# Performance work log

Hardware: AMD Instinct MI355X
Metric: run time of the kernel (lower is better)

The kernel has to match this reference:

```python
import jax, jax.numpy as jnp
import numpy as np

N_Q_HEADS = 16
N_KV_HEADS = 4
HEAD_DIM = 128
SLIDING_WINDOW = 1024
ROPE_BASE = 1024


def _rope_tables(L, dim):
    # half-truncate RoPE: first dim//4 freqs geometric, next dim//4 zero
    freqs = (1.0 / ROPE_BASE) ** jnp.linspace(0.0, 1.0, num=dim // 4)
    freqs = jnp.concatenate([freqs, jnp.zeros(dim // 4, dtype=freqs.dtype)])
    theta = jnp.arange(L, dtype=jnp.float32)[:, None] * freqs[None, :]  # (L, dim/2)
    cos = jnp.cos(theta)[None, :, None, :]  # (1, L, 1, dim/2)
    sin = jnp.sin(theta)[None, :, None, :]
    return cos, sin


def _rotate(x, cos, sin):
    # x: (B, L, H, D)
    x1, x2 = jnp.split(x, 2, axis=-1)
    return jnp.concatenate([x1 * cos + x2 * sin, -x1 * sin + x2 * cos], axis=-1)


def setup_inputs() -> dict:
    key = jax.random.key(0)
    k1, k2, k3, k4 = jax.random.split(key, 4)
    B, L, D = 1, 2048, 2048
    qkv_dim = (N_Q_HEADS + 2 * N_KV_HEADS) * HEAD_DIM  # 3072
    return {
        "x": jax.random.normal(k1, (B, L, D), dtype=jnp.float32),
        "Wqkv": jax.random.normal(k2, (D, qkv_dim), dtype=jnp.float32) * (D ** -0.5),
        "Wo": jax.random.normal(k3, (N_Q_HEADS * HEAD_DIM, D), dtype=jnp.float32) * ((N_Q_HEADS * HEAD_DIM) ** -0.5),
        "s": jax.random.normal(k4, (1, N_Q_HEADS), dtype=jnp.float32) * 0.1,
    }


def reference(x, Wqkv, Wo, s):
    B, L, D = x.shape
    H, QM, hd = N_KV_HEADS, N_Q_HEADS // N_KV_HEADS, HEAD_DIM

    proj = x @ Wqkv  # (B, L, (Hq + 2*Hkv) * hd)
    q, k, v = jnp.split(proj, (N_Q_HEADS * hd, (N_Q_HEADS + N_KV_HEADS) * hd), axis=-1)

    cos, sin = _rope_tables(L, hd)
    q = _rotate(q.reshape(B, L, -1, hd), cos, sin).reshape(B, L, H, QM, hd)
    k = _rotate(k.reshape(B, L, H, hd), cos, sin)
    v = v.reshape(B, L, H, hd)

    sm_scale = 1.0 / jnp.sqrt(jnp.float32(hd))
    q_pos = jnp.arange(L)[None, :, None]
    k_pos = jnp.arange(L)[None, None, :]
    causal = q_pos >= k_pos                       # (1, L, L)
    window = q_pos < k_pos + SLIDING_WINDOW       # index % 2 == 0 -> window active
    mask = causal & window

    # (B, H, M, Lq, Lk) attention logits
    attn = jnp.einsum("bqhmd,bkhd->bhmqk", q, k) * sm_scale
    # NOTE: faithful to source: -inf placed WHERE mask is True
    attn = jnp.where(mask, -jnp.inf, attn)

    sink = jnp.broadcast_to(s.reshape(B, H, QM, 1, 1), (B, H, QM, L, 1))
    w = jax.nn.softmax(jnp.concatenate([attn, sink], axis=-1), axis=-1)[..., :-1]

    out = jnp.einsum("bhmqk,bkhd->bqhmd", w, v).reshape(B, L, -1)
    return out @ Wo
```

## Files before the change

kernel.cpp:

```cpp
#include <hip/hip_runtime.h>
#include <hip/hip_bf16.h>
#include <math.h>

typedef __bf16 bf16;
typedef __bf16 bf16x8 __attribute__((ext_vector_type(8)));
typedef __bf16 bf16x4v __attribute__((ext_vector_type(4)));
typedef short s16x4 __attribute__((ext_vector_type(4)));
typedef float f32x4 __attribute__((ext_vector_type(4)));

#define GLD16(gp, lp) __builtin_amdgcn_global_load_lds( \
    (__attribute__((address_space(1))) void*)(void*)(gp), \
    (__attribute__((address_space(3))) void*)(lp), 16, 0, 0)

#define L_SEQ 2048
#define D_MODEL 2048
#define QKV_N 3072
#define HD 128
#define QSCALE 0.1275310242959836f
#define LOG2E 1.4426950408889634f

__global__ __launch_bounds__(256) void prep(const float* __restrict__ x,
                                            const float* __restrict__ Wqkv,
                                            const float* __restrict__ Wo,
                                            bf16* __restrict__ xb,
                                            bf16* __restrict__ wqkvT,
                                            bf16* __restrict__ woT) {
    __shared__ float tile[32][33];
    int bid = blockIdx.x;
    if (bid < 4096) {
        int idx = (bid * 256 + threadIdx.x) * 4;
        float4 f = *(const float4*)(x + idx);
        bf16x4v o;
        o.x = (bf16)f.x; o.y = (bf16)f.y; o.z = (bf16)f.z; o.w = (bf16)f.w;
        *(bf16x4v*)(xb + idx) = o;
        return;
    }
    bid -= 4096;
    const float* src; bf16* dst; long ld_s, ld_d; int bx, by;
    if (bid < 6144) { bx = bid % 96; by = bid / 96; src = Wqkv; dst = wqkvT; ld_s = QKV_N; ld_d = D_MODEL; }
    else { bid -= 6144; bx = bid & 63; by = bid >> 6; src = Wo; dst = woT; ld_s = D_MODEL; ld_d = D_MODEL; }
    const int tx = threadIdx.x & 31, ty = threadIdx.x >> 5;
    const long c = bx * 32 + tx, r0 = by * 32;
#pragma unroll
    for (int i = 0; i < 4; ++i)
        tile[ty + i * 8][tx] = src[(r0 + ty + i * 8) * ld_s + c];
    __syncthreads();
    const long c0 = bx * 32;
#pragma unroll
    for (int i = 0; i < 4; ++i)
        dst[(c0 + ty + i * 8) * ld_d + r0 + tx] = (bf16)tile[tx][ty + i * 8];
}

__global__ __launch_bounds__(256) void gemm_qkv(const bf16* __restrict__ A,
                                                const bf16* __restrict__ Bt,
                                                bf16* __restrict__ Qb,
                                                bf16* __restrict__ Kb,
                                                bf16* __restrict__ Vtb) {
    constexpr int K = D_MODEL;
    __shared__ __align__(16) bf16 As[128 * 32];
    __shared__ __align__(16) bf16 Bs[128 * 32];
    const int tid = threadIdx.x;
    const int wid = tid >> 6, lane = tid & 63;
    const int quad = lane >> 4, l15 = lane & 15;
    const int wm = wid & 1, wn = wid >> 1;
    const int head = blockIdx.x;
    const long m0 = (long)blockIdx.y * 128, n0 = (long)head * 128;

    const int srow = wid * 32 + (lane >> 2);
    const int scol = ((lane & 3) ^ ((lane >> 3) & 3)) * 8;

    f32x4 acc[4][4];
#pragma unroll
    for (int i = 0; i < 4; ++i)
#pragma unroll
        for (int j = 0; j < 4; ++j) acc[i][j] = (f32x4){0.f, 0.f, 0.f, 0.f};

    const bf16* Ap  = A  + (m0 + srow) * K + scol;
    const bf16* Ap2 = Ap + (long)16 * K;
    const bf16* Bp  = Bt + (n0 + srow) * K + scol;
    const bf16* Bp2 = Bp + (long)16 * K;
    bf16* lA  = &As[(wid * 32) * 32];
    bf16* lA2 = &As[(wid * 32 + 16) * 32];
    bf16* lB  = &Bs[(wid * 32) * 32];
    bf16* lB2 = &Bs[(wid * 32 + 16) * 32];

    const int rsw = ((l15 >> 1) & 3);

    for (int k0 = 0; k0 < K; k0 += 32) {
        GLD16(Ap + k0, lA);
        GLD16(Ap2 + k0, lA2);
        GLD16(Bp + k0, lB);
        GLD16(Bp2 + k0, lB2);
        __syncthreads();
        bf16x8 af[4], bfr[4];
#pragma unroll
        for (int i = 0; i < 4; ++i)
            af[i] = *(const bf16x8*)&As[(wm * 64 + i * 16 + l15) * 32 + (quad ^ rsw) * 8];
#pragma unroll
        for (int j = 0; j < 4; ++j)
            bfr[j] = *(const bf16x8*)&Bs[(j * 32 + wn * 16 + l15) * 32 + (quad ^ rsw) * 8];
#pragma unroll
        for (int i = 0; i < 4; ++i)
#pragma unroll
            for (int j = 0; j < 4; ++j)
                acc[i][j] = __builtin_amdgcn_mfma_f32_16x16x32_bf16(af[i], bfr[j], acc[i][j], 0, 0, 0);
        __syncthreads();
    }

    const int d0 = wn * 16 + l15;
    if (head < 20) {
        const float freq = exp2f((float)d0 * (-10.0f / 31.0f));
        const float sc = head < 16 ? QSCALE : 1.0f;
        bf16* dst = head < 16 ? Qb + (long)head * L_SEQ * HD
                              : Kb + (long)(head - 16) * L_SEQ * HD;
#pragma unroll
        for (int i = 0; i < 4; ++i) {
            const long mb = m0 + wm * 64 + i * 16 + quad * 4;
#pragma unroll
            for (int r = 0; r < 4; ++r) {
                const long row = mb + r;
                float sn, cs;
                sincosf((float)row * freq, &sn, &cs);
                const float x1 = acc[i][0][r], x2 = acc[i][2][r];
                bf16* p = dst + row * HD + d0;
                p[0]  = (bf16)((x1 * cs + x2 * sn) * sc);
                p[64] = (bf16)((x2 * cs - x1 * sn) * sc);
                p[32] = (bf16)(acc[i][1][r] * sc);
                p[96] = (bf16)(acc[i][3][r] * sc);
            }
        }
    } else {
        bf16* dst = Vtb + (long)(head - 20) * HD * L_SEQ;
#pragma unroll
        for (int i = 0; i < 4; ++i) {
            const long m = m0 + wm * 64 + i * 16 + quad * 4;
#pragma unroll
            for (int j = 0; j < 4; ++j) {
                const int d = j * 32 + d0;
                bf16x4v vv;
#pragma unroll
                for (int r = 0; r < 4; ++r) vv[r] = (bf16)acc[i][j][r];
                *(bf16x4v*)(dst + (long)d * L_SEQ + m) = vv;
            }
        }
    }
}

__global__ __launch_bounds__(256) void gemm_bt(const bf16* __restrict__ A,
                                               const bf16* __restrict__ Bt,
                                               float* __restrict__ C,
                                               int M, int N, int K) {
    __shared__ __align__(16) bf16 As[128 * 32];
    __shared__ __align__(16) bf16 Bs[128 * 32];
    const int tid = threadIdx.x;
    const int wid = tid >> 6, lane = tid & 63;
    const int quad = lane >> 4, l15 = lane & 15;
    const int wm = wid & 1, wn = wid >> 1;
    const long m0 = (long)blockIdx.y * 128, n0 = (long)blockIdx.x * 128;

    const int srow = wid * 32 + (lane >> 2);
    const int scol = ((lane & 3) ^ ((lane >> 3) & 3)) * 8;

    f32x4 acc[4][4];
#pragma unroll
    for (int i = 0; i < 4; ++i)
#pragma unroll
        for (int j = 0; j < 4; ++j) acc[i][j] = (f32x4){0.f, 0.f, 0.f, 0.f};

    const bf16* Ap  = A  + (m0 + srow) * K + scol;
    const bf16* Ap2 = Ap + (long)16 * K;
    const bf16* Bp  = Bt + (n0 + srow) * K + scol;
    const bf16* Bp2 = Bp + (long)16 * K;
    bf16* lA  = &As[(wid * 32) * 32];
    bf16* lA2 = &As[(wid * 32 + 16) * 32];
    bf16* lB  = &Bs[(wid * 32) * 32];
    bf16* lB2 = &Bs[(wid * 32 + 16) * 32];

    const int rsw = ((l15 >> 1) & 3);

    for (int k0 = 0; k0 < K; k0 += 32) {
        GLD16(Ap + k0, lA);
        GLD16(Ap2 + k0, lA2);
        GLD16(Bp + k0, lB);
        GLD16(Bp2 + k0, lB2);
        __syncthreads();
        bf16x8 af[4], bfr[4];
#pragma unroll
        for (int i = 0; i < 4; ++i)
            af[i] = *(const bf16x8*)&As[(wm * 64 + i * 16 + l15) * 32 + (quad ^ rsw) * 8];
#pragma unroll
        for (int j = 0; j < 4; ++j)
            bfr[j] = *(const bf16x8*)&Bs[(wn * 64 + j * 16 + l15) * 32 + (quad ^ rsw) * 8];
#pragma unroll
        for (int i = 0; i < 4; ++i)
#pragma unroll
            for (int j = 0; j < 4; ++j)
                acc[i][j] = __builtin_amdgcn_mfma_f32_16x16x32_bf16(af[i], bfr[j], acc[i][j], 0, 0, 0);
        __syncthreads();
    }
#pragma unroll
    for (int i = 0; i < 4; ++i)
#pragma unroll
        for (int j = 0; j < 4; ++j) {
            long m = m0 + wm * 64 + i * 16 + quad * 4;
            long n = n0 + wn * 64 + j * 16 + l15;
#pragma unroll
            for (int r = 0; r < 4; ++r)
                C[(m + r) * (long)N + n] = acc[i][j][r];
        }
}

__global__ __launch_bounds__(512, 2) void attn_kernel(const bf16* __restrict__ Qb,
                                                      const bf16* __restrict__ Kb,
                                                      const bf16* __restrict__ Vtb,
                                                      const float* __restrict__ sink,
                                                      bf16* __restrict__ Ob) {
    __shared__ __align__(1024) char smem[131072];

    const int bid = blockIdx.x;
    const int t  = bid & 15;
    const int hq = bid >> 4;
    const int h = hq >> 2;
    const int q0 = t * 128;
    const int tid = threadIdx.x;
    const int wid8 = tid >> 6;
    const int g = wid8 >> 2;
    const int w = wid8 & 3;
    const int lane = tid & 63;
    const int quad = lane >> 4, l15 = lane & 15;

    const bf16* Qg = Qb + (long)hq * L_SEQ * HD;
    const bf16* Kg = Kb + (long)h * L_SEQ * HD;
    const bf16* Vg = Vtb + (long)h * HD * L_SEQ;

    bf16x8 qb[2][4];
#pragma unroll
    for (int rf = 0; rf < 2; ++rf)
#pragma unroll
        for (int kkd = 0; kkd < 4; ++kkd)
            qb[rf][kkd] = *(const bf16x8*)(Qg + (long)(q0 + w * 32 + rf * 16 + l15) * HD
                                              + kkd * 32 + quad * 8);

    f32x4 oaccT[2][8];
#pragma unroll
    for (int rf = 0; rf < 2; ++rf)
#pragma unroll
        for (int j = 0; j < 8; ++j) oaccT[rf][j] = (f32x4){0.f, 0.f, 0.f, 0.f};
    float lacc[2] = {0.f, 0.f};

    const int locnt = (2 * t - 14 > 0) ? (2 * t - 14) : 0;
    const int n = locnt + 32 - 2 * t;
    const int iters = (n + 1) >> 1;

    auto stage = [&](int it2, int buf) {
        const int i = 2 * it2 + g;
        if (i >= n) return;
        const int kt = (i < locnt) ? i : (2 * t + (i - locnt));
        const int k0 = kt * 64;
        bf16* Ksb  = (bf16*)(smem + g * 65536 + buf * 32768);
        bf16* Vtsb = (bf16*)(smem + g * 65536 + buf * 32768 + 16384);
#pragma unroll
        for (int ii = 0; ii < 4; ++ii) {
            int rowb = w * 16 + ii * 4;
            int row = rowb + quad;
            GLD16(Kg + (long)(k0 + row) * HD + ((l15 ^ (row & 7)) * 8), &Ksb[rowb * 128]);
        }
#pragma unroll
        for (int ii = 0; ii < 4; ++ii) {
            int rowb = w * 32 + ii * 8;
            int row = rowb + (lane >> 3);
            GLD16(Vg + (long)row * L_SEQ + k0 + (((lane & 7) ^ (row & 7)) * 8), &Vtsb[rowb * 64]);
        }
    };

    stage(0, 0);

    for (int it = 0; it < iters; ++it) {
        __syncthreads();
        if (it + 1 < iters) stage(it + 1, (it + 1) & 1);

        const int i = 2 * it + g;
        if (i >= n) continue;
        const int kt = (i < locnt) ? i : (2 * t + (i - locnt));
        const int k0 = kt * 64;
        const bf16* Ks  = (const bf16*)(smem + g * 65536 + (it & 1) * 32768);
        const bf16* Vts = (const bf16*)(smem + g * 65536 + (it & 1) * 32768 + 16384);

        f32x4 sacc[2][4];
#pragma unroll
        for (int kb = 0; kb < 4; ++kb) {
            bf16x8 ka[4];
#pragma unroll
            for (int kkd = 0; kkd < 4; ++kkd)
                ka[kkd] = *(const bf16x8*)&Ks[(kb * 16 + l15) * 128 +
                                              (((kkd * 4 + quad) ^ (l15 & 7)) * 8)];
#pragma unroll
            for (int rf = 0; rf < 2; ++rf) {
                f32x4 acc = (f32x4){0.f, 0.f, 0.f, 0.f};
#pragma unroll
                for (int kkd = 0; kkd < 4; ++kkd)
                    acc = __builtin_amdgcn_mfma_f32_16x16x32_bf16(ka[kkd], qb[rf][kkd], acc, 0, 0, 0);
                sacc[rf][kb] = acc;
            }
        }

        const bool bnd = (kt == 2 * t) || (kt == 2 * t + 1) ||
                         (kt == 2 * t - 15) || (kt == 2 * t - 16);
        s16x4 pb[2][4];
#pragma unroll
        for (int rf = 0; rf < 2; ++rf) {
            const int qq = q0 + w * 32 + rf * 16 + l15;
#pragma unroll
            for (int kb = 0; kb < 4; ++kb) {
#pragma unroll
                for (int r = 0; r < 4; ++r) {
                    float v = sacc[rf][kb][r];
                    if (bnd) {
                        const int kk = k0 + kb * 16 + quad * 4 + r;
                        if (!((kk > qq) || (kk <= qq - 1024))) v = -1e30f;
                    }
                    const float p = exp2f(v);
                    lacc[rf] += p;
                    bf16 hp = (bf16)p;
                    pb[rf][kb][r] = __builtin_bit_cast(short, hp);
                }
            }
        }

#pragma unroll
        for (int j = 0; j < 8; ++j) {
            const int drow = j * 16 + l15;
#pragma unroll
            for (int kq = 0; kq < 4; ++kq) {
                const int pc = ((kq * 2 + (quad >> 1)) ^ (l15 & 7));
                s16x4 va = *(const s16x4*)((const char*)&Vts[drow * 64] + pc * 16 + (quad & 1) * 8);
#pragma unroll
                for (int rf = 0; rf < 2; ++rf)
                    oaccT[rf][j] = __builtin_amdgcn_mfma_f32_16x16x16bf16_1k(
                        va, pb[rf][kq], oaccT[rf][j], 0, 0, 0);
            }
        }
    }

#pragma unroll
    for (int rf = 0; rf < 2; ++rf) {
        lacc[rf] += __shfl_xor(lacc[rf], 16, 64);
        lacc[rf] += __shfl_xor(lacc[rf], 32, 64);
    }

    __syncthreads();
    float* Obuf = (float*)smem;
    float* lbuf = (float*)(smem + 67584);
    if (g == 1) {
#pragma unroll
        for (int rf = 0; rf < 2; ++rf) {
            const int ql = w * 32 + rf * 16 + l15;
#pragma unroll
            for (int j = 0; j < 8; ++j)
                *(f32x4*)&Obuf[ql * 132 + j * 16 + quad * 4] = oaccT[rf][j];
            if (quad == 0) lbuf[ql] = lacc[rf];
        }
    }
    __syncthreads();
    if (g == 0) {
        const float sv2 = sink[hq] * LOG2E;
#pragma unroll
        for (int rf = 0; rf < 2; ++rf) {
            const int ql = w * 32 + rf * 16 + l15;
            const float ltot = lacc[rf] + lbuf[ql] + exp2f(sv2);
            const float inv = 1.0f / ltot;
            bf16* dst = Ob + (long)(q0 + ql) * D_MODEL + hq * HD;
#pragma unroll
            for (int j = 0; j < 8; ++j) {
                f32x4 o2 = *(const f32x4*)&Obuf[ql * 132 + j * 16 + quad * 4];
                bf16x4v ov;
#pragma unroll
                for (int r = 0; r < 4; ++r)
                    ov[r] = (bf16)((oaccT[rf][j][r] + o2[r]) * inv);
                *(bf16x4v*)(dst + j * 16 + quad * 4) = ov;
            }
        }
    }
}

extern "C" void kernel_launch(void* const* d_in, const int* in_sizes, int n_in,
                              void* d_out, int out_size, void* d_ws, size_t ws_size,
                              hipStream_t stream) {
    (void)in_sizes; (void)n_in; (void)out_size; (void)ws_size;
    const float* x    = (const float*)d_in[0];
    const float* Wqkv = (const float*)d_in[1];
    const float* Wo   = (const float*)d_in[2];
    const float* s    = (const float*)d_in[3];
    float* out = (float*)d_out;

    char* ws = (char*)d_ws;
    bf16* xb    = (bf16*)ws;  ws += (size_t)D_MODEL * D_MODEL * 2;
    bf16* wqkvT = (bf16*)ws;  ws += (size_t)QKV_N * D_MODEL * 2;
    bf16* woT   = (bf16*)ws;  ws += (size_t)D_MODEL * D_MODEL * 2;
    bf16* Qb    = (bf16*)ws;  ws += (size_t)16 * L_SEQ * HD * 2;
    bf16* Kb    = (bf16*)ws;  ws += (size_t)4 * L_SEQ * HD * 2;
    bf16* Vtb   = (bf16*)ws;  ws += (size_t)4 * HD * L_SEQ * 2;
    bf16* attnb = (bf16*)ws;  ws += (size_t)L_SEQ * D_MODEL * 2;

    prep<<<14336, 256, 0, stream>>>(x, Wqkv, Wo, xb, wqkvT, woT);

    gemm_qkv<<<dim3(QKV_N / 128, L_SEQ / 128), 256, 0, stream>>>(
        xb, wqkvT, Qb, Kb, Vtb);

    attn_kernel<<<256, 512, 0, stream>>>(Qb, Kb, Vtb, s, attnb);

    gemm_bt<<<dim3(D_MODEL / 128, L_SEQ / 128), 256, 0, stream>>>(
        attnb, woT, out, L_SEQ, D_MODEL, D_MODEL);
}
```

Baseline: 244.5 us.

## Split-K the output projection GEMM and read attention K directly from global

The output projection GEMM is split into two K halves over a third grid dimension, writing fp32 partials into reused workspace, followed by a small reduction kernel. This doubles the block count (256 to 512) to fill more CUs, at the cost of extra partial-buffer traffic and a launch. Separately, the attention kernel stops staging K tiles in LDS and loads them straight from global memory, halving shared memory (which may raise occupancy) but relying on cache for K reuse. The workspace is rearranged so the partials overlay the no-longer-needed xb/wqkvT buffers.

```diff
diff --git a/kernel.cpp b/kernel.cpp
--- a/kernel.cpp
+++ b/kernel.cpp
@@ -146,10 +146,10 @@
     }
 }
 
-__global__ __launch_bounds__(256) void gemm_bt(const bf16* __restrict__ A,
-                                               const bf16* __restrict__ Bt,
-                                               float* __restrict__ C,
-                                               int M, int N, int K) {
+__global__ __launch_bounds__(256) void gemm_bt_splitk(const bf16* __restrict__ A,
+                                                      const bf16* __restrict__ Bt,
+                                                      float* __restrict__ Cp,
+                                                      int M, int N, int K) {
     __shared__ __align__(16) bf16 As[128 * 32];
     __shared__ __align__(16) bf16 Bs[128 * 32];
     const int tid = threadIdx.x;
@@ -157,6 +157,8 @@
     const int quad = lane >> 4, l15 = lane & 15;
     const int wm = wid & 1, wn = wid >> 1;
     const long m0 = (long)blockIdx.y * 128, n0 = (long)blockIdx.x * 128;
+    const int kz0 = blockIdx.z * (K >> 1), kz1 = kz0 + (K >> 1);
+    float* C = Cp + (long)blockIdx.z * M * N;
 
     const int srow = wid * 32 + (lane >> 2);
     const int scol = ((lane & 3) ^ ((lane >> 3) & 3)) * 8;
@@ -178,7 +180,7 @@
 
     const int rsw = ((l15 >> 1) & 3);
 
-    for (int k0 = 0; k0 < K; k0 += 32) {
+    for (int k0 = kz0; k0 < kz1; k0 += 32) {
         GLD16(Ap + k0, lA);
         GLD16(Ap2 + k0, lA2);
         GLD16(Bp + k0, lB);
@@ -210,12 +212,21 @@
         }
 }
 
+__global__ __launch_bounds__(256) void reduce2(const float* __restrict__ p,
+                                               float* __restrict__ out, int n) {
+    const int idx = (blockIdx.x * 256 + threadIdx.x) * 4;
+    if (idx >= n) return;
+    f32x4 a = *(const f32x4*)(p + idx);
+    f32x4 b = *(const f32x4*)(p + n + idx);
+    *(f32x4*)(out + idx) = a + b;
+}
+
 __global__ __launch_bounds__(512, 2) void attn_kernel(const bf16* __restrict__ Qb,
                                                       const bf16* __restrict__ Kb,
                                                       const bf16* __restrict__ Vtb,
                                                       const float* __restrict__ sink,
                                                       bf16* __restrict__ Ob) {
-    __shared__ __align__(1024) char smem[131072];
+    __shared__ __align__(1024) char smem[68608];
 
     const int bid = blockIdx.x;
     const int t  = bid & 15;
@@ -252,19 +263,12 @@
     const int n = locnt + 32 - 2 * t;
     const int iters = (n + 1) >> 1;
 
-    auto stage = [&](int it2, int buf) {
+    auto stageV = [&](int it2, int buf) {
         const int i = 2 * it2 + g;
         if (i >= n) return;
         const int kt = (i < locnt) ? i : (2 * t + (i - locnt));
         const int k0 = kt * 64;
-        bf16* Ksb  = (bf16*)(smem + g * 65536 + buf * 32768);
-        bf16* Vtsb = (bf16*)(smem + g * 65536 + buf * 32768 + 16384);
-#pragma unroll
-        for (int ii = 0; ii < 4; ++ii) {
-            int rowb = w * 16 + ii * 4;
-            int row = rowb + quad;
-            GLD16(Kg + (long)(k0 + row) * HD + ((l15 ^ (row & 7)) * 8), &Ksb[rowb * 128]);
-        }
+        bf16* Vtsb = (bf16*)(smem + g * 32768 + buf * 16384);
 #pragma unroll
         for (int ii = 0; ii < 4; ++ii) {
             int rowb = w * 32 + ii * 8;
@@ -273,18 +277,18 @@
         }
     };
 
-    stage(0, 0);
+    stageV(0, 0);
 
     for (int it = 0; it < iters; ++it) {
         __syncthreads();
-        if (it + 1 < iters) stage(it + 1, (it + 1) & 1);
+        if (it + 1 < iters) stageV(it + 1, (it + 1) & 1);
 
         const int i = 2 * it + g;
         if (i >= n) continue;
         const int kt = (i < locnt) ? i : (2 * t + (i - locnt));
         const int k0 = kt * 64;
-        const bf16* Ks  = (const bf16*)(smem + g * 65536 + (it & 1) * 32768);
-        const bf16* Vts = (const bf16*)(smem + g * 65536 + (it & 1) * 32768 + 16384);
+        const bf16* Vts = (const bf16*)(smem + g * 32768 + (it & 1) * 16384);
+        const bf16* Kt = Kg + (long)k0 * HD;
 
         f32x4 sacc[2][4];
 #pragma unroll
@@ -292,8 +296,7 @@
             bf16x8 ka[4];
 #pragma unroll
             for (int kkd = 0; kkd < 4; ++kkd)
-                ka[kkd] = *(const bf16x8*)&Ks[(kb * 16 + l15) * 128 +
-                                              (((kkd * 4 + quad) ^ (l15 & 7)) * 8)];
+                ka[kkd] = *(const bf16x8*)(Kt + (long)(kb * 16 + l15) * HD + kkd * 32 + quad * 8);
 #pragma unroll
             for (int rf = 0; rf < 2; ++rf) {
                 f32x4 acc = (f32x4){0.f, 0.f, 0.f, 0.f};
@@ -394,13 +397,14 @@
     float* out = (float*)d_out;
 
     char* ws = (char*)d_ws;
-    bf16* xb    = (bf16*)ws;  ws += (size_t)D_MODEL * D_MODEL * 2;
-    bf16* wqkvT = (bf16*)ws;  ws += (size_t)QKV_N * D_MODEL * 2;
-    bf16* woT   = (bf16*)ws;  ws += (size_t)D_MODEL * D_MODEL * 2;
-    bf16* Qb    = (bf16*)ws;  ws += (size_t)16 * L_SEQ * HD * 2;
-    bf16* Kb    = (bf16*)ws;  ws += (size_t)4 * L_SEQ * HD * 2;
-    bf16* Vtb   = (bf16*)ws;  ws += (size_t)4 * HD * L_SEQ * 2;
-    bf16* attnb = (bf16*)ws;  ws += (size_t)L_SEQ * D_MODEL * 2;
+    bf16* xb    = (bf16*)ws;
+    bf16* wqkvT = (bf16*)(ws + 8388608);
+    bf16* Qb    = (bf16*)(ws + 8388608 + 12582912);
+    bf16* Kb    = (bf16*)((char*)Qb + 8388608);
+    bf16* Vtb   = (bf16*)((char*)Kb + 2097152);
+    bf16* woT   = (bf16*)((char*)Vtb + 2097152);
+    bf16* attnb = (bf16*)((char*)woT + 8388608);
+    float* part = (float*)ws;
 
     prep<<<14336, 256, 0, stream>>>(x, Wqkv, Wo, xb, wqkvT, woT);
 
@@ -409,6 +413,9 @@
 
     attn_kernel<<<256, 512, 0, stream>>>(Qb, Kb, Vtb, s, attnb);
 
-    gemm_bt<<<dim3(D_MODEL / 128, L_SEQ / 128), 256, 0, stream>>>(
-        attnb, woT, out, L_SEQ, D_MODEL, D_MODEL);
-}
+    gemm_bt_splitk<<<dim3(D_MODEL / 128, L_SEQ / 128, 2), 256, 0, stream>>>(
+        attnb, woT, part, L_SEQ, D_MODEL, D_MODEL);
+
+    reduce2<<<(D_MODEL * L_SEQ) / 1024, 256, 0, stream>>>(
+        part, out, L_SEQ * D_MODEL);
+}
```

Result: slower. 285.4 us (+16.7%).
